# Kernel optimization log

Measured on AMD Instinct MI355X. Metric: run time of the kernel, lower is better.

Reference implementation:

```python
import jax, jax.numpy as jnp
import numpy as np

RADIUS = 8
EPSILON = 0.01


def _diff_x(x, r):
    left = x[..., r:2 * r + 1, :]
    middle = x[..., 2 * r + 1:, :] - x[..., :-2 * r - 1, :]
    right = x[..., -1:, :] - x[..., -2 * r - 1:-r - 1, :]
    return jnp.concatenate([left, middle, right], axis=-2)


def _diff_y(x, r):
    left = x[..., r:2 * r + 1]
    middle = x[..., 2 * r + 1:] - x[..., :-2 * r - 1]
    right = x[..., -1:] - x[..., -2 * r - 1:-r - 1]
    return jnp.concatenate([left, middle, right], axis=-1)


def box_filter(x, r):
    # x: (N, C, H, W) -> windowed mean over (2r+1)x(2r+1) with reflect padding
    x = jnp.pad(x, ((0, 0), (0, 0), (r, r), (r, r)), mode='reflect')
    x = jnp.cumsum(x, axis=-2)
    x = _diff_x(x, r)
    x = jnp.cumsum(x, axis=-1)
    x = _diff_y(x, r)
    return x[..., r:-r, r:-r] / float((2 * r + 1) ** 2)


def setup_inputs() -> dict:
    key = jax.random.key(0)
    k1, k2 = jax.random.split(key)
    B, C, H, W = 4, 3, 1024, 1024
    I = jax.random.uniform(k1, (B, C, H, W), dtype=jnp.float32)
    p = jax.random.uniform(k2, (B, 1, H, W), dtype=jnp.float32)
    return {"I": I, "p": p}


def reference(I, p) -> jnp.ndarray:
    r, eps = RADIUS, EPSILON
    B, C, H, W = I.shape

    mean_I = box_filter(I, r)                     # (B,C,H,W)
    mean_p = box_filter(p, r)                     # (B,1,H,W)
    mean_Ip = box_filter(I * p, r)                # (B,C,H,W)
    cov_Ip = mean_Ip - mean_I * mean_p            # (B,C,H,W)

    # second moments: (B,C,C,H,W) via reshape to (B*C, C, H, W) for the box filter
    II = I[:, :, None] * I[:, None]               # (B,C,C,H,W)
    mean_II = box_filter(II.reshape(B * C, C, H, W), r).reshape(B, C, C, H, W)
    cov_II = mean_II - mean_I[:, :, None] * mean_I[:, None]

    eye = jnp.eye(C, dtype=I.dtype).reshape(1, C, C, 1, 1)
    S = cov_II + eps * eye                        # (B,C,C,H,W)

    # per-pixel CxC solve: move pixel dims to batch
    S_px = jnp.transpose(S, (0, 3, 4, 1, 2))      # (B,H,W,C,C)
    rhs = jnp.transpose(cov_Ip, (0, 2, 3, 1))[..., None]  # (B,H,W,C,1)
    a = jnp.linalg.solve(S_px, rhs)[..., 0]       # (B,H,W,C)
    a = jnp.transpose(a, (0, 3, 1, 2))            # (B,C,H,W)

    a_mean_I = jnp.einsum('bchw,bchw->bhw', a, mean_I)
    b = mean_p - a_mean_I[:, None]                # (B,1,H,W)

    mean_a = box_filter(a, r)
    mean_b = box_filter(b, r)

    q = jnp.einsum('bchw,bchw->bhw', mean_a, I) + mean_b[:, 0]
    return q[:, None]                             # (B,1,H,W)
```

## Files before the change

### kernel.cpp

```cpp
#include <hip/hip_runtime.h>

#define HH 1024
#define WW 1024
#define NB 4
#define RR 8
#define NCH1 13
#define NCH2 4
#define VSEG 8
#define NSEG (HH / VSEG)
#define NXCD 8
#define NBLK1 (NB * NSEG)
#define CPX1 (NBLK1 / NXCD)
#define LDSW1 1040
#define TW 512
#define NWS (WW / TW)
#define NBLK2 (NB * NSEG * NWS)
#define CPX2 (NBLK2 / NXCD)
#define LDSW2 544
#define INV_AREA (1.0f/289.0f)
#define EPS_REG 0.01f

typedef float f4 __attribute__((ext_vector_type(4)));
typedef _Float16 h4 __attribute__((ext_vector_type(4)));
typedef float f2 __attribute__((ext_vector_type(2)));
typedef _Float16 h2 __attribute__((ext_vector_type(2)));

__device__ __forceinline__ int refl(int j, int n) {
    int k = j < 0 ? -j : j;
    return k >= n ? 2 * n - 2 - k : k;
}

__device__ __forceinline__ void derived13(f4 i0, f4 i1, f4 i2, f4 pp, f4* d) {
    d[0] = i0; d[1] = i1; d[2] = i2; d[3] = pp;
    d[4] = i0 * pp; d[5] = i1 * pp; d[6] = i2 * pp;
    d[7] = i0 * i0; d[8] = i0 * i1; d[9] = i0 * i2;
    d[10] = i1 * i1; d[11] = i1 * i2; d[12] = i2 * i2;
}

__global__ __launch_bounds__(256, 2) void gf_stage1(
    const float* __restrict__ I, const float* __restrict__ P,
    _Float16* __restrict__ A, _Float16* __restrict__ Bc)
{
    __shared__ float lds[NCH1][LDSW1];
    const int tid = threadIdx.x;
    const int logical = (blockIdx.x & (NXCD - 1)) * CPX1 + (blockIdx.x >> 3);
    const int bz = logical / NSEG;
    const int y0 = (logical % NSEG) * VSEG;
    const int c0 = 4 * tid;
    const float* Ib = I + (size_t)bz * 3 * HH * WW;
    const float* Pb = P + (size_t)bz * HH * WW;

    f4 vs[NCH1];
    #pragma unroll
    for (int ch = 0; ch < NCH1; ++ch) { vs[ch] = (f4){0.f, 0.f, 0.f, 0.f}; }

    for (int dy = -RR; dy <= RR; ++dy) {
        int row = refl(y0 + dy, HH);
        size_t rb = (size_t)row * WW + c0;
        f4 i0 = *(const f4*)(Ib + rb);
        f4 i1 = *(const f4*)(Ib + (size_t)HH * WW + rb);
        f4 i2 = *(const f4*)(Ib + (size_t)2 * HH * WW + rb);
        f4 pp = *(const f4*)(Pb + rb);
        f4 d[NCH1]; derived13(i0, i1, i2, pp, d);
        #pragma unroll
        for (int ch = 0; ch < NCH1; ++ch) vs[ch] += d[ch];
    }

    for (int y = y0; y < y0 + VSEG; ++y) {
        #pragma unroll
        for (int ch = 0; ch < NCH1; ++ch)
            *(f4*)&lds[ch][8 + c0] = vs[ch];
        if (tid <= 2) {
            #pragma unroll
            for (int j = 0; j < 4; ++j) {
                int c = c0 + j;
                if (c >= 1 && c <= 8) {
                    #pragma unroll
                    for (int ch = 0; ch < NCH1; ++ch) lds[ch][8 - c] = vs[ch][j];
                }
            }
        }
        if (tid >= 253) {
            #pragma unroll
            for (int j = 0; j < 4; ++j) {
                int c = c0 + j;
                if (c >= 1015 && c <= 1022) {
                    #pragma unroll
                    for (int ch = 0; ch < NCH1; ++ch) lds[ch][1032 + (1022 - c)] = vs[ch][j];
                }
            }
        }
        const bool upd = (y + 1 < y0 + VSEG);
        f4 ai0, ai1, ai2, ap, si0, si1, si2, sp;
        if (upd) {
            int ra = refl(y + 1 + RR, HH);
            int rs = refl(y - RR, HH);
            size_t rba = (size_t)ra * WW + c0;
            size_t rbs = (size_t)rs * WW + c0;
            ai0 = *(const f4*)(Ib + rba);
            ai1 = *(const f4*)(Ib + (size_t)HH * WW + rba);
            ai2 = *(const f4*)(Ib + (size_t)2 * HH * WW + rba);
            ap  = *(const f4*)(Pb + rba);
            si0 = *(const f4*)(Ib + rbs);
            si1 = *(const f4*)(Ib + (size_t)HH * WW + rbs);
            si2 = *(const f4*)(Ib + (size_t)2 * HH * WW + rbs);
            sp  = *(const f4*)(Pb + rbs);
        }
        __syncthreads();

        f4 m[NCH1];
        #pragma unroll
        for (int ch = 0; ch < NCH1; ++ch) {
            float vv[20];
            #pragma unroll
            for (int k = 0; k < 5; ++k)
                ((f4*)vv)[k] = *(const f4*)&lds[ch][c0 + 4 * k];
            float s = (((vv[0]+vv[1])+(vv[2]+vv[3])) + ((vv[4]+vv[5])+(vv[6]+vv[7])))
                    + (((vv[8]+vv[9])+(vv[10]+vv[11])) + ((vv[12]+vv[13])+(vv[14]+vv[15])))
                    + vv[16];
            f4 mm;
            mm[0] = s;
            s += vv[17] - vv[0]; mm[1] = s;
            s += vv[18] - vv[1]; mm[2] = s;
            s += vv[19] - vv[2]; mm[3] = s;
            m[ch] = mm * INV_AREA;
        }

        f4 oa0, oa1, oa2, ob;
        #pragma unroll
        for (int j = 0; j < 4; ++j) {
            float m0 = m[0][j], m1 = m[1][j], m2 = m[2][j], m3 = m[3][j];
            float r0 = m[4][j] - m0 * m3;
            float r1 = m[5][j] - m1 * m3;
            float r2 = m[6][j] - m2 * m3;
            float S00 = m[7][j]  - m0 * m0 + EPS_REG;
            float S01 = m[8][j]  - m0 * m1;
            float S02 = m[9][j]  - m0 * m2;
            float S11 = m[10][j] - m1 * m1 + EPS_REG;
            float S12 = m[11][j] - m1 * m2;
            float S22 = m[12][j] - m2 * m2 + EPS_REG;
            float A0 = S11 * S22 - S12 * S12;
            float B0 = S02 * S12 - S01 * S22;
            float C0 = S01 * S12 - S02 * S11;
            float D0 = S00 * S22 - S02 * S02;
            float E0 = S01 * S02 - S00 * S12;
            float F0 = S00 * S11 - S01 * S01;
            float det = S00 * A0 + S01 * B0 + S02 * C0;
            float inv = 1.0f / det;
            float a0 = (A0 * r0 + B0 * r1 + C0 * r2) * inv;
            float a1 = (B0 * r0 + D0 * r1 + E0 * r2) * inv;
            float a2 = (C0 * r0 + E0 * r1 + F0 * r2) * inv;
            float bb = m3 - (a0 * m0 + a1 * m1 + a2 * m2);
            oa0[j] = a0; oa1[j] = a1; oa2[j] = a2; ob[j] = bb;
        }
        size_t obase = (size_t)y * WW + c0;
        *(h4*)(A + (size_t)(bz * 3 + 0) * HH * WW + obase) = __builtin_convertvector(oa0, h4);
        *(h4*)(A + (size_t)(bz * 3 + 1) * HH * WW + obase) = __builtin_convertvector(oa1, h4);
        *(h4*)(A + (size_t)(bz * 3 + 2) * HH * WW + obase) = __builtin_convertvector(oa2, h4);
        *(h4*)(Bc + (size_t)bz * HH * WW + obase) = __builtin_convertvector(ob, h4);
        __syncthreads();

        if (upd) {
            f4 d[NCH1];
            derived13(ai0, ai1, ai2, ap, d);
            #pragma unroll
            for (int ch = 0; ch < NCH1; ++ch) vs[ch] += d[ch];
            derived13(si0, si1, si2, sp, d);
            #pragma unroll
            for (int ch = 0; ch < NCH1; ++ch) vs[ch] -= d[ch];
        }
    }
}

__device__ __forceinline__ f2 hwin2(const float* ldsrow, int c0) {
    const f2* wp = (const f2*)(ldsrow + c0);
    f2 w0 = wp[0], w1 = wp[1], w2 = wp[2], w3 = wp[3];
    f2 w4 = wp[4], w5 = wp[5], w6 = wp[6], w7 = wp[7], w8 = wp[8];
    f2 e = ((w0 + w1) + (w2 + w3)) + ((w4 + w5) + (w6 + w7));
    float s0 = e[0] + e[1] + w8[0];
    float s1 = s0 - w0[0] + w8[1];
    f2 r; r[0] = s0 * INV_AREA; r[1] = s1 * INV_AREA;
    return r;
}

__global__ __launch_bounds__(256, 2) void gf_stage2(
    const float* __restrict__ I, const _Float16* __restrict__ A,
    const _Float16* __restrict__ Bc, float* __restrict__ Q)
{
    __shared__ float lds[NCH2][LDSW2];
    const int tid = threadIdx.x;
    const int logical = (blockIdx.x & (NXCD - 1)) * CPX2 + (blockIdx.x >> 3);
    const int strip = logical / NSEG;
    const int y0 = (logical % NSEG) * VSEG;
    const int bz = strip >> 1;
    const int wstart = (strip & 1) * TW;
    const int c0 = 2 * tid;
    const int gc = wstart + c0;
    const _Float16* A0p = A + (size_t)(bz * 3 + 0) * HH * WW;
    const _Float16* A1p = A + (size_t)(bz * 3 + 1) * HH * WW;
    const _Float16* A2p = A + (size_t)(bz * 3 + 2) * HH * WW;
    const _Float16* Bp  = Bc + (size_t)bz * HH * WW;
    const float* Ib  = I + (size_t)bz * 3 * HH * WW;

    const bool isHalo = tid < 16;
    const int hraw = (tid < 8) ? (wstart - 8 + tid) : (wstart + TW + (tid - 8));
    const int hg = refl(hraw, WW);
    const int hpos = (tid < 8) ? tid : (8 + TW + (tid - 8));

    f2 vs[NCH2];
    float hs[NCH2];
    #pragma unroll
    for (int ch = 0; ch < NCH2; ++ch) { vs[ch] = (f2){0.f, 0.f}; hs[ch] = 0.f; }

    for (int dy = -RR; dy <= RR; ++dy) {
        int row = refl(y0 + dy, HH);
        size_t rb = (size_t)row * WW;
        vs[0] += __builtin_convertvector(*(const h2*)(A0p + rb + gc), f2);
        vs[1] += __builtin_convertvector(*(const h2*)(A1p + rb + gc), f2);
        vs[2] += __builtin_convertvector(*(const h2*)(A2p + rb + gc), f2);
        vs[3] += __builtin_convertvector(*(const h2*)(Bp + rb + gc), f2);
        if (isHalo) {
            hs[0] += (float)A0p[rb + hg];
            hs[1] += (float)A1p[rb + hg];
            hs[2] += (float)A2p[rb + hg];
            hs[3] += (float)Bp[rb + hg];
        }
    }

    for (int y = y0; y < y0 + VSEG; ++y) {
        #pragma unroll
        for (int ch = 0; ch < NCH2; ++ch)
            *(f2*)&lds[ch][8 + c0] = vs[ch];
        if (isHalo) {
            #pragma unroll
            for (int ch = 0; ch < NCH2; ++ch) lds[ch][hpos] = hs[ch];
        }
        const bool upd = (y + 1 < y0 + VSEG);
        f2 aa0, aa1, aa2, ab, sa0, sa1, sa2, sb;
        float ha0, ha1, ha2, hab, hb0, hb1, hb2, hbb;
        size_t rbq = (size_t)y * WW;
        f2 i0 = *(const f2*)(Ib + rbq + gc);
        f2 i1 = *(const f2*)(Ib + (size_t)HH * WW + rbq + gc);
        f2 i2 = *(const f2*)(Ib + (size_t)2 * HH * WW + rbq + gc);
        if (upd) {
            int ra = refl(y + 1 + RR, HH);
            int rs = refl(y - RR, HH);
            size_t rba = (size_t)ra * WW;
            size_t rbs = (size_t)rs * WW;
            aa0 = __builtin_convertvector(*(const h2*)(A0p + rba + gc), f2);
            aa1 = __builtin_convertvector(*(const h2*)(A1p + rba + gc), f2);
            aa2 = __builtin_convertvector(*(const h2*)(A2p + rba + gc), f2);
            ab  = __builtin_convertvector(*(const h2*)(Bp + rba + gc), f2);
            sa0 = __builtin_convertvector(*(const h2*)(A0p + rbs + gc), f2);
            sa1 = __builtin_convertvector(*(const h2*)(A1p + rbs + gc), f2);
            sa2 = __builtin_convertvector(*(const h2*)(A2p + rbs + gc), f2);
            sb  = __builtin_convertvector(*(const h2*)(Bp + rbs + gc), f2);
            if (isHalo) {
                ha0 = (float)A0p[rba + hg]; ha1 = (float)A1p[rba + hg];
                ha2 = (float)A2p[rba + hg]; hab = (float)Bp[rba + hg];
                hb0 = (float)A0p[rbs + hg]; hb1 = (float)A1p[rbs + hg];
                hb2 = (float)A2p[rbs + hg]; hbb = (float)Bp[rbs + hg];
            }
        }
        __syncthreads();

        f2 m[NCH2];
        #pragma unroll
        for (int ch = 0; ch < NCH2; ++ch)
            m[ch] = hwin2(&lds[ch][0], c0);

        f2 qv = m[0] * i0 + m[1] * i1 + m[2] * i2 + m[3];
        *(f2*)(Q + (size_t)bz * HH * WW + rbq + gc) = qv;
        __syncthreads();

        if (upd) {
            vs[0] += aa0 - sa0;
            vs[1] += aa1 - sa1;
            vs[2] += aa2 - sa2;
            vs[3] += ab - sb;
            if (isHalo) {
                hs[0] += ha0 - hb0; hs[1] += ha1 - hb1;
                hs[2] += ha2 - hb2; hs[3] += hab - hbb;
            }
        }
    }
}

extern "C" void kernel_launch(void* const* d_in, const int* in_sizes, int n_in,
                              void* d_out, int out_size, void* d_ws, size_t ws_size,
                              hipStream_t stream) {
    const float* I = (const float*)d_in[0];
    const float* P = (const float*)d_in[1];
    float* Q = (float*)d_out;
    _Float16* A = (_Float16*)d_ws;
    _Float16* Bc = A + (size_t)NB * 3 * HH * WW;
    gf_stage1<<<NBLK1, 256, 0, stream>>>(I, P, A, Bc);
    gf_stage2<<<NBLK2, 256, 0, stream>>>(I, A, Bc, Q);
}
```

Measured before the change: 86.62 us.

## Halve stage-1 row segment and remap block-to-XCD assignment by batch

Stage 1 now processes 4 rows per block instead of 8, doubling its block count to raise parallelism. Both stages remap block indices so that each pair of XCDs serves one batch image, with the two halves of the rows split between them, and stage 2 interleaves the two column strips within a rank. This is meant to improve L2 locality per XCD and load balance. Shorter segments in stage 1 raise the relative cost of the 17-row vertical window prefill per block.

```diff
diff --git a/kernel.cpp b/kernel.cpp
--- a/kernel.cpp
+++ b/kernel.cpp
@@ -6,16 +6,15 @@
 #define RR 8
 #define NCH1 13
 #define NCH2 4
-#define VSEG 8
-#define NSEG (HH / VSEG)
 #define NXCD 8
-#define NBLK1 (NB * NSEG)
-#define CPX1 (NBLK1 / NXCD)
+#define VSEG1 4
+#define NSEG1 (HH / VSEG1)
+#define NBLK1 (NB * NSEG1)
 #define LDSW1 1040
+#define VSEG2 8
+#define NSEG2 (HH / VSEG2)
 #define TW 512
-#define NWS (WW / TW)
-#define NBLK2 (NB * NSEG * NWS)
-#define CPX2 (NBLK2 / NXCD)
+#define NBLK2 (NB * NSEG2 * 2)
 #define LDSW2 544
 #define INV_AREA (1.0f/289.0f)
 #define EPS_REG 0.01f
@@ -36,6 +35,7 @@
     d[7] = i0 * i0; d[8] = i0 * i1; d[9] = i0 * i2;
     d[10] = i1 * i1; d[11] = i1 * i2; d[12] = i2 * i2;
 }
+
 
 __global__ __launch_bounds__(256, 2) void gf_stage1(
     const float* __restrict__ I, const float* __restrict__ P,
@@ -43,9 +43,11 @@
 {
     __shared__ float lds[NCH1][LDSW1];
     const int tid = threadIdx.x;
-    const int logical = (blockIdx.x & (NXCD - 1)) * CPX1 + (blockIdx.x >> 3);
-    const int bz = logical / NSEG;
-    const int y0 = (logical % NSEG) * VSEG;
+    const int xcd = blockIdx.x & (NXCD - 1);
+    const int rank = blockIdx.x >> 3;
+    const int bz = xcd >> 1;
+    const int seg = (xcd & 1) * 128 + rank;
+    const int y0 = seg * VSEG1;
     const int c0 = 4 * tid;
     const float* Ib = I + (size_t)bz * 3 * HH * WW;
     const float* Pb = P + (size_t)bz * HH * WW;
@@ -66,7 +68,7 @@
         for (int ch = 0; ch < NCH1; ++ch) vs[ch] += d[ch];
     }
 
-    for (int y = y0; y < y0 + VSEG; ++y) {
+    for (int y = y0; y < y0 + VSEG1; ++y) {
         #pragma unroll
         for (int ch = 0; ch < NCH1; ++ch)
             *(f4*)&lds[ch][8 + c0] = vs[ch];
@@ -90,7 +92,7 @@
                 }
             }
         }
-        const bool upd = (y + 1 < y0 + VSEG);
+        const bool upd = (y + 1 < y0 + VSEG1);
         f4 ai0, ai1, ai2, ap, si0, si1, si2, sp;
         if (upd) {
             int ra = refl(y + 1 + RR, HH);
@@ -189,11 +191,12 @@
 {
     __shared__ float lds[NCH2][LDSW2];
     const int tid = threadIdx.x;
-    const int logical = (blockIdx.x & (NXCD - 1)) * CPX2 + (blockIdx.x >> 3);
-    const int strip = logical / NSEG;
-    const int y0 = (logical % NSEG) * VSEG;
-    const int bz = strip >> 1;
-    const int wstart = (strip & 1) * TW;
+    const int xcd = blockIdx.x & (NXCD - 1);
+    const int rank = blockIdx.x >> 3;
+    const int bz = xcd >> 1;
+    const int seg = (xcd & 1) * 64 + (rank >> 1);
+    const int y0 = seg * VSEG2;
+    const int wstart = (rank & 1) * TW;
     const int c0 = 2 * tid;
     const int gc = wstart + c0;
     const _Float16* A0p = A + (size_t)(bz * 3 + 0) * HH * WW;
@@ -227,7 +230,7 @@
         }
     }
 
-    for (int y = y0; y < y0 + VSEG; ++y) {
+    for (int y = y0; y < y0 + VSEG2; ++y) {
         #pragma unroll
         for (int ch = 0; ch < NCH2; ++ch)
             *(f2*)&lds[ch][8 + c0] = vs[ch];
@@ -235,7 +238,7 @@
             #pragma unroll
             for (int ch = 0; ch < NCH2; ++ch) lds[ch][hpos] = hs[ch];
         }
-        const bool upd = (y + 1 < y0 + VSEG);
+        const bool upd = (y + 1 < y0 + VSEG2);
         f2 aa0, aa1, aa2, ab, sa0, sa1, sa2, sb;
         float ha0, ha1, ha2, hab, hb0, hb1, hb2, hbb;
         size_t rbq = (size_t)y * WW;
```

Result: faster. 81.89 us, median of 2 (-5.5%).
